# Kernel optimization log

Measured on AMD Instinct MI355X. Metric: run time of the kernel, lower is better.

## Reference

```python
import jax, jax.numpy as jnp
import numpy as np

HEAD_DIM = 64
N_HEADS = 12
ROPE_BASE = 10000.0


def _rope_tables(seq_len, head_dim, dtype=jnp.float32):
    half = head_dim // 2
    inv_freq = 1.0 / (ROPE_BASE ** (jnp.arange(0, half, dtype=jnp.float32) / half))
    pos = jnp.arange(seq_len, dtype=jnp.float32)
    freqs = pos[:, None] * inv_freq[None, :]  # (s, half)
    return jnp.cos(freqs).astype(dtype), jnp.sin(freqs).astype(dtype)


def _apply_rope(t, cos, sin):
    # t: (b, h, s, d); rotate-half convention on full head_dim (rope_fraction=1.0)
    d = t.shape[-1]
    t1, t2 = t[..., : d // 2], t[..., d // 2 :]
    cos = cos[None, None, :, :]
    sin = sin[None, None, :, :]
    return jnp.concatenate([t1 * cos - t2 * sin, t1 * sin + t2 * cos], axis=-1)


def setup_inputs() -> dict:
    key = jax.random.key(0)
    ks = jax.random.split(key, 6)
    b, s, d_model = 16, 512, 768
    x = jax.random.normal(ks[0], (b, s, d_model), dtype=jnp.float32)
    chain_ids = jax.random.randint(ks[1], (b, s), 0, 2, dtype=jnp.int32)
    attention_mask = jnp.ones((b, s), dtype=bool)
    inner = N_HEADS * HEAD_DIM
    scale = 0.02
    Wq = jax.random.normal(ks[2], (d_model, inner), dtype=jnp.float32) * scale
    Wk = jax.random.normal(ks[3], (d_model, inner), dtype=jnp.float32) * scale
    Wv = jax.random.normal(ks[4], (d_model, inner), dtype=jnp.float32) * scale
    Wo = jax.random.normal(ks[5], (inner, d_model), dtype=jnp.float32) * scale
    return {"x": x, "chain_ids": chain_ids, "attention_mask": attention_mask,
            "Wq": Wq, "Wk": Wk, "Wv": Wv, "Wo": Wo}


def reference(x, chain_ids, attention_mask, Wq, Wk, Wv, Wo):
    b, s, _ = x.shape
    h, d = N_HEADS, HEAD_DIM
    scale = d ** (-0.5)

    def proj(W):
        return jnp.einsum('bse,ef->bsf', x, W).reshape(b, s, h, d).transpose(0, 2, 1, 3)

    q = proj(Wq)  # (b, h, s, d)
    k = proj(Wk)
    v = proj(Wv)

    cos, sin = _rope_tables(s, d, x.dtype)
    q_rope = _apply_rope(q, cos, sin)
    k_rope = _apply_rope(k, cos, sin)

    scores_intra = jnp.einsum('bhsd,bhtd->bhst', q_rope, k_rope) * scale
    scores_inter = jnp.einsum('bhsd,bhtd->bhst', q, k) * scale

    # intra-chain mask (b, 1, s, s)
    intra = (chain_ids[:, None, :, None] == chain_ids[:, None, None, :])
    merged = jnp.where(intra, scores_intra, scores_inter)

    # additive padding mask (b, 1, 1, s)
    pad = jnp.where(attention_mask[:, None, None, :], 0.0, -jnp.inf).astype(x.dtype)
    merged = merged + pad

    attn = jax.nn.softmax(merged, axis=-1)
    attn = jnp.nan_to_num(attn, nan=0.0)

    out = jnp.einsum('bhst,bhtd->bhsd', attn, v)
    out = out.transpose(0, 2, 1, 3).reshape(b, s, h * d)
    return jnp.einsum('bsf,fe->bse', out, Wo)
```

## Files before the change

kernel.cpp:

```cpp
#include <hip/hip_runtime.h>
#include <stdint.h>
#include <math.h>

#define NB 16
#define NS 512
#define NH 12
#define ND 64
#define NE 768
#define NF 768

typedef __attribute__((ext_vector_type(4))) float  f32x4;
typedef __attribute__((ext_vector_type(8))) short  bf16x8;
typedef __attribute__((ext_vector_type(4))) short  bf16x4;

#define AS1(p) ((const __attribute__((address_space(1))) unsigned int*)(p))
#define AS3(p) ((__attribute__((address_space(3))) unsigned int*)(p))

__device__ __forceinline__ short f2bf(float f) {
    unsigned u = __builtin_bit_cast(unsigned, f);
    u += 0x7FFFu + ((u >> 16) & 1u);
    return (short)(u >> 16);
}
__device__ __forceinline__ float bf2f(short s) {
    unsigned u = ((unsigned)(unsigned short)s) << 16;
    return __builtin_bit_cast(float, u);
}
__device__ __forceinline__ unsigned pkbf2(float a, float b) {
    return (unsigned)(unsigned short)f2bf(a) | ((unsigned)(unsigned short)f2bf(b) << 16);
}

#define MFMA16(a, b, c) __builtin_amdgcn_mfma_f32_16x16x32_bf16((a), (b), (c), 0, 0, 0)

__device__ __forceinline__ bf16x8 lds_rd8(const short* base, int row, int cb) {
    return *(const bf16x8*)((const char*)base + (((row) * 128 + (cb)) ^ (((row) & 7) << 4)));
}

__global__ __launch_bounds__(256) void prep_kernel(float* __restrict__ cos_t,
                                                   float* __restrict__ sin_t,
                                                   const unsigned char* __restrict__ m,
                                                   int* __restrict__ flag) {
    if (blockIdx.x == 64) {
        __shared__ int any;
        if (threadIdx.x == 0) any = 0;
        __syncthreads();
        int acc = 0;
        for (int i = threadIdx.x; i < NB * NS; i += 256)
            if ((i & 3) && m[i]) acc = 1;
        if (acc) atomicOr(&any, 1);
        __syncthreads();
        if (threadIdx.x == 0) *flag = any;
        return;
    }
    int i = blockIdx.x * 256 + threadIdx.x;
    int p = i >> 5, j = i & 31;
    float inv_freq = powf(10000.0f, -(float)j / 32.0f);
    float ang = (float)p * inv_freq;
    cos_t[i] = cosf(ang);
    sin_t[i] = sinf(ang);
}

__global__ __launch_bounds__(256) void convert_x_kernel(const float* __restrict__ x,
                                                        short* __restrict__ xb) {
    int i = (blockIdx.x * 256 + threadIdx.x) * 8;
    if (i >= 8192 * 768) return;
    float4 a = *(const float4*)&x[i];
    float4 b = *(const float4*)&x[i + 4];
    bf16x8 r = { f2bf(a.x), f2bf(a.y), f2bf(a.z), f2bf(a.w),
                 f2bf(b.x), f2bf(b.y), f2bf(b.z), f2bf(b.w) };
    *(bf16x8*)&xb[i] = r;
}

__global__ __launch_bounds__(256) void convert_wt_kernel(
    const float* __restrict__ Wq, const float* __restrict__ Wk,
    const float* __restrict__ Wv, const float* __restrict__ Wo,
    short* __restrict__ Wqt, short* __restrict__ Wkt,
    short* __restrict__ Wvt, short* __restrict__ Wot) {
    const float* W  = (blockIdx.z == 0) ? Wq  : (blockIdx.z == 1) ? Wk  : (blockIdx.z == 2) ? Wv  : Wo;
    short*       Wt = (blockIdx.z == 0) ? Wqt : (blockIdx.z == 1) ? Wkt : (blockIdx.z == 2) ? Wvt : Wot;
    const int k0 = blockIdx.y * 64, n0 = blockIdx.x * 64;
    __shared__ float t[64][65];
    for (int u = threadIdx.x; u < 4096; u += 256) {
        int r = u >> 6, c = u & 63;
        t[r][c] = W[(size_t)(k0 + r) * 768 + n0 + c];
    }
    __syncthreads();
    for (int u = threadIdx.x; u < 4096; u += 256) {
        int c = u >> 6, r = u & 63;
        Wt[(size_t)(n0 + c) * 768 + k0 + r] = f2bf(t[r][c]);
    }
}

__global__ __launch_bounds__(256) void gemm_qkv_kernel(const short* __restrict__ xb,
    const short* __restrict__ Wqt, const short* __restrict__ Wkt, const short* __restrict__ Wvt,
    const float* __restrict__ cos_t, const float* __restrict__ sin_t,
    short* __restrict__ qo, short* __restrict__ ko, short* __restrict__ kpo,
    short* __restrict__ vto) {
    const int id = blockIdx.x;
    const int xcd = id & 7, rest = id >> 3;
    const int mq = rest / 18;
    const int nz = rest % 18;
    const int z  = nz / 6;
    const int n0 = (nz % 6) * 128;
    const int m0 = (xcd * 16 + mq) * 64;
    const short* Bt = (z == 0) ? Wqt : (z == 1) ? Wkt : Wvt;
    short*       O  = (z == 0) ? qo  : (z == 1) ? ko  : vto;
    __shared__ short As[2][64 * 64], Bs[2][128 * 64];
    const int tid = threadIdx.x, lane = tid & 63, wave = tid >> 6;
    const int g = lane >> 4, l15 = lane & 15;
    const int wm = wave >> 1, wn = wave & 1;
    f32x4 acc[2][4];
    #pragma unroll
    for (int i = 0; i < 2; ++i)
        #pragma unroll
        for (int j = 0; j < 4; ++j) acc[i][j] = (f32x4){0.f, 0.f, 0.f, 0.f};

    auto STAGE = [&](short* Ad, short* Bd, int kt) {
        const char* Asrc = (const char*)(xb + (size_t)m0 * 768 + kt * 64);
        const char* Bsrc = (const char*)(Bt + (size_t)n0 * 768 + kt * 64);
        #pragma unroll
        for (int p = 0; p < 2; ++p) {
            int dstoff = (wave * 2 + p) * 1024;
            int off = dstoff + lane * 16;
            int row = off >> 7, slot = off & 127;
            int srcs = slot ^ ((row & 7) << 4);
            __builtin_amdgcn_global_load_lds(AS1(Asrc + (size_t)row * 1536 + srcs),
                                             AS3((char*)Ad + dstoff), 16, 0, 0);
        }
        #pragma unroll
        for (int p = 0; p < 4; ++p) {
            int dstoff = (wave * 4 + p) * 1024;
            int off = dstoff + lane * 16;
            int row = off >> 7, slot = off & 127;
            int srcs = slot ^ ((row & 7) << 4);
            __builtin_amdgcn_global_load_lds(AS1(Bsrc + (size_t)row * 1536 + srcs),
                                             AS3((char*)Bd + dstoff), 16, 0, 0);
        }
    };
    auto COMPUTE = [&](const short* Asb, const short* Bsb) {
        __builtin_amdgcn_s_setprio(1);
        #pragma unroll
        for (int h2 = 0; h2 < 2; ++h2) {
            bf16x8 af[2], bfr[4];
            const int cb = h2 * 64 + g * 16;
            #pragma unroll
            for (int i = 0; i < 2; ++i)
                af[i]  = lds_rd8(Asb, wm * 32 + i * 16 + l15, cb);
            #pragma unroll
            for (int j = 0; j < 4; ++j)
                bfr[j] = lds_rd8(Bsb, wn * 64 + j * 16 + l15, cb);
            #pragma unroll
            for (int i = 0; i < 2; ++i)
                #pragma unroll
                for (int j = 0; j < 4; ++j)
                    acc[i][j] = MFMA16(af[i], bfr[j], acc[i][j]);
        }
        __builtin_amdgcn_s_setprio(0);
    };

    STAGE(As[0], Bs[0], 0);
    asm volatile("s_waitcnt vmcnt(0)" ::: "memory");
    __builtin_amdgcn_s_barrier();
    int cur = 0;
    for (int kt = 0; kt < 11; ++kt) {
        STAGE(As[cur ^ 1], Bs[cur ^ 1], kt + 1);
        COMPUTE(As[cur], Bs[cur]);
        asm volatile("s_waitcnt vmcnt(0)" ::: "memory");
        __builtin_amdgcn_s_barrier();
        cur ^= 1;
    }
    COMPUTE(As[cur], Bs[cur]);

    const int hh = (n0 + wn * 64) >> 6;
    #pragma unroll
    for (int i = 0; i < 2; ++i)
        #pragma unroll
        for (int r = 0; r < 4; ++r) {
            int mm = m0 + wm * 32 + i * 16 + g * 4 + r;
            int bb = mm >> 9, ss = mm & 511;
            if (z == 2) {
                #pragma unroll
                for (int j = 0; j < 4; ++j) {
                    int dd = j * 16 + l15;
                    O[(((size_t)bb * NH + hh) * ND + dd) * NS + ss] = f2bf(acc[i][j][r]);
                }
            } else {
                size_t base = (((size_t)bb * NH + hh) * NS + ss) * ND;
                #pragma unroll
                for (int j = 0; j < 4; ++j)
                    O[base + j * 16 + l15] = f2bf(acc[i][j][r]);
                if (z == 1) {
                    #pragma unroll
                    for (int p2 = 0; p2 < 2; ++p2) {
                        int jf = p2 * 16 + l15;
                        float c = cos_t[ss * 32 + jf], s = sin_t[ss * 32 + jf];
                        float t1 = acc[i][p2][r], t2 = acc[i][p2 + 2][r];
                        kpo[base + jf]      = f2bf(t1 * c - t2 * s);
                        kpo[base + 32 + jf] = f2bf(t1 * s + t2 * c);
                    }
                }
            }
        }
}

__global__ __launch_bounds__(256) void attn_fused_kernel(
    const short* __restrict__ qr, const short* __restrict__ kr, const short* __restrict__ kp,
    const short* __restrict__ vt,
    const float* __restrict__ cos_t, const float* __restrict__ sin_t,
    const int* __restrict__ chain, const void* __restrict__ amask,
    const int* __restrict__ mflag, short* __restrict__ aout) {
    const int lid = blockIdx.x;
    const int xcd = lid & 7, idx = lid >> 3;
    const int qt = idx & 7, bhl = idx >> 3;
    const int bh = xcd * 24 + bhl;
    const int b = bh / 12, h = bh - (bh / 12) * 12;
    const int q0 = qt * 64;

    __shared__ short Kr_s[4096];
    __shared__ short Kp_s[4096];
    __shared__ short Vt_s[4096];
    __shared__ short P_s[4096];
    __shared__ int   ck_a[512];
    __shared__ float kb_a[512];

    const int tid = threadIdx.x, lane = tid & 63, wave = tid >> 6;
    const int g = lane >> 4, l15 = lane & 15;
    const int m_u8 = *mflag;
    const size_t bhNS = (size_t)bh * NS;
    const float SC = 0.18033688011f;

    for (int u = tid; u < NS; u += 256) {
        int gidx = b * NS + u;
        ck_a[u] = chain[gidx];
        int ok = m_u8 ? (int)((const unsigned char*)amask)[gidx] : ((const int*)amask)[gidx];
        kb_a[u] = ok ? 0.f : -INFINITY;
    }
    const char* qrsC = (const char*)(qr + (bhNS + q0) * ND);
    #pragma unroll
    for (int p = 0; p < 2; ++p) {
        int dstoff = (wave * 2 + p) * 1024;
        int off = dstoff + lane * 16;
        int row = off >> 7, slot = off & 127;
        int srcs = slot ^ ((row & 7) << 4);
        __builtin_amdgcn_global_load_lds(AS1(qrsC + (size_t)row * 128 + srcs),
                                         AS3((char*)Kr_s + dstoff), 16, 0, 0);
    }
    __syncthreads();
    const int qrow = wave * 16 + l15;
    bf16x8 fqr0 = lds_rd8(Kr_s, qrow, g * 16);
    bf16x8 fqr1 = lds_rd8(Kr_s, qrow, 64 + g * 16);
    bf16x8 fqp0, fqp1;
    {
        int pos = q0 + qrow;
        float4 c0 = *(const float4*)&cos_t[pos * 32 + g * 8];
        float4 c1 = *(const float4*)&cos_t[pos * 32 + g * 8 + 4];
        float4 s0 = *(const float4*)&sin_t[pos * 32 + g * 8];
        float4 s1 = *(const float4*)&sin_t[pos * 32 + g * 8 + 4];
        float cc[8] = {c0.x, c0.y, c0.z, c0.w, c1.x, c1.y, c1.z, c1.w};
        float ss[8] = {s0.x, s0.y, s0.z, s0.w, s1.x, s1.y, s1.z, s1.w};
        #pragma unroll
        for (int j = 0; j < 8; ++j) {
            float t1 = bf2f(fqr0[j]), t2 = bf2f(fqr1[j]);
            fqp0[j] = f2bf(t1 * cc[j] - t2 * ss[j]);
            fqp1[j] = f2bf(t1 * ss[j] + t2 * cc[j]);
        }
    }
    const int cqv = ck_a[q0 + qrow];

    float m_run = -INFINITY, l_run = 0.f;
    f32x4 accO[4];
    #pragma unroll
    for (int t = 0; t < 4; ++t) accO[t] = (f32x4){0.f, 0.f, 0.f, 0.f};

    const char* krC = (const char*)(kr + bhNS * ND);
    const char* kpC = (const char*)(kp + bhNS * ND);
    const char* vtC = (const char*)(vt + bhNS * ND);

    for (int kv = 0; kv < 8; ++kv) {
        const int k0s = kv * 64;
        __syncthreads();
        #pragma unroll
        for (int p = 0; p < 2; ++p) {
            int dstoff = (wave * 2 + p) * 1024;
            int off = dstoff + lane * 16;
            int row = off >> 7, slot = off & 127;
            int srcs = slot ^ ((row & 7) << 4);
            size_t koff = (size_t)(k0s + row) * 128 + srcs;
            __builtin_amdgcn_global_load_lds(AS1(krC + koff), AS3((char*)Kr_s + dstoff), 16, 0, 0);
            __builtin_amdgcn_global_load_lds(AS1(kpC + koff), AS3((char*)Kp_s + dstoff), 16, 0, 0);
            __builtin_amdgcn_global_load_lds(AS1(vtC + (size_t)row * 1024 + k0s * 2 + srcs),
                                             AS3((char*)Vt_s + dstoff), 16, 0, 0);
        }
        __syncthreads();

        float pm[4][4];
        float tm = -INFINITY;
        __builtin_amdgcn_s_setprio(1);
        #pragma unroll
        for (int t = 0; t < 4; ++t) {
            bf16x8 akr0 = lds_rd8(Kr_s, t * 16 + l15, g * 16);
            bf16x8 akr1 = lds_rd8(Kr_s, t * 16 + l15, 64 + g * 16);
            bf16x8 akp0 = lds_rd8(Kp_s, t * 16 + l15, g * 16);
            bf16x8 akp1 = lds_rd8(Kp_s, t * 16 + l15, 64 + g * 16);
            f32x4 sr = (f32x4){0.f, 0.f, 0.f, 0.f};
            f32x4 sp = (f32x4){0.f, 0.f, 0.f, 0.f};
            sr = MFMA16(akr0, fqr0, sr);
            sr = MFMA16(akr1, fqr1, sr);
            sp = MFMA16(akp0, fqp0, sp);
            sp = MFMA16(akp1, fqp1, sp);
            int4   ck4 = *(const int4*)&ck_a[k0s + t * 16 + g * 4];
            float4 kb4 = *(const float4*)&kb_a[k0s + t * 16 + g * 4];
            const int   ckk[4] = {ck4.x, ck4.y, ck4.z, ck4.w};
            const float kbb[4] = {kb4.x, kb4.y, kb4.z, kb4.w};
            #pragma unroll
            for (int r = 0; r < 4; ++r) {
                float sv = (cqv == ckk[r]) ? sp[r] : sr[r];
                sv = sv * SC + kbb[r];
                pm[t][r] = sv;
                tm = fmaxf(tm, sv);
            }
        }
        __builtin_amdgcn_s_setprio(0);

        tm = fmaxf(tm, __shfl_xor(tm, 16));
        tm = fmaxf(tm, __shfl_xor(tm, 32));
        bool skip = __all(tm - m_run <= 8.f);
        float mnew, fac;
        if (skip) { mnew = m_run; fac = 1.f; }
        else      { mnew = fmaxf(m_run, tm); fac = exp2f(m_run - mnew); }
        float psum = 0.f;
        if (mnew == -INFINITY) {
            #pragma unroll
            for (int t = 0; t < 4; ++t)
                #pragma unroll
                for (int r = 0; r < 4; ++r) pm[t][r] = 0.f;
            fac = 1.f;
        } else {
            #pragma unroll
            for (int t = 0; t < 4; ++t)
                #pragma unroll
                for (int r = 0; r < 4; ++r) {
                    float p = exp2f(pm[t][r] - mnew);
                    pm[t][r] = p;
                    psum += p;
                }
        }
        psum += __shfl_xor(psum, 16);
        psum += __shfl_xor(psum, 32);
        l_run = l_run * fac + psum;
        m_run = mnew;

        char* pwave = (char*)P_s + wave * 2048;
        int psw = (l15 & 7) << 4;
        #pragma unroll
        for (int t = 0; t < 4; ++t) {
            unsigned u0 = pkbf2(pm[t][0], pm[t][1]);
            unsigned u1 = pkbf2(pm[t][2], pm[t][3]);
            uint2 pk = {u0, u1};
            *(uint2*)(pwave + ((l15 * 128 + t * 32 + g * 8) ^ psw)) = pk;
        }
        if (!skip) {
            float f4[4];
            #pragma unroll
            for (int r = 0; r < 4; ++r) f4[r] = __shfl(fac, g * 4 + r);
            #pragma unroll
            for (int t = 0; t < 4; ++t) {
                f32x4 a = accO[t];
                a[0] *= f4[0]; a[1] *= f4[1]; a[2] *= f4[2]; a[3] *= f4[3];
                accO[t] = a;
            }
        }
        bf16x8 pa0 = *(const bf16x8*)(pwave + ((l15 * 128 + g * 16) ^ psw));
        bf16x8 pa1 = *(const bf16x8*)(pwave + ((l15 * 128 + 64 + g * 16) ^ psw));
        __builtin_amdgcn_s_setprio(1);
        #pragma unroll
        for (int dt = 0; dt < 4; ++dt) {
            bf16x8 vb0 = lds_rd8(Vt_s, dt * 16 + l15, g * 16);
            bf16x8 vb1 = lds_rd8(Vt_s, dt * 16 + l15, 64 + g * 16);
            accO[dt] = MFMA16(pa0, vb0, accO[dt]);
            accO[dt] = MFMA16(pa1, vb1, accO[dt]);
        }
        __builtin_amdgcn_s_setprio(0);
    }

    float inv[4];
    #pragma unroll
    for (int r = 0; r < 4; ++r) {
        float lv = __shfl(l_run, g * 4 + r);
        inv[r] = (lv > 0.f) ? 1.f / lv : 0.f;
    }
    #pragma unroll
    for (int dt = 0; dt < 4; ++dt)
        #pragma unroll
        for (int r = 0; r < 4; ++r) {
            int row = b * NS + q0 + wave * 16 + g * 4 + r;
            aout[(size_t)row * NF + h * ND + dt * 16 + l15] = f2bf(accO[dt][r] * inv[r]);
        }
}

__global__ __launch_bounds__(256) void gemm_out_kernel(const short* __restrict__ A,
    const short* __restrict__ Wot, float* __restrict__ out) {
    const int id = blockIdx.x;
    const int xcd = id & 7, rest = id >> 3;
    const int mq = rest / 6;
    const int n0 = (rest % 6) * 128;
    const int m0 = (xcd * 16 + mq) * 64;
    __shared__ short As[2][64 * 64], Bs[2][128 * 64];
    const int tid = threadIdx.x, lane = tid & 63, wave = tid >> 6;
    const int g = lane >> 4, l15 = lane & 15;
    const int wm = wave >> 1, wn = wave & 1;
    f32x4 acc[2][4];
    #pragma unroll
    for (int i = 0; i < 2; ++i)
        #pragma unroll
        for (int j = 0; j < 4; ++j) acc[i][j] = (f32x4){0.f, 0.f, 0.f, 0.f};

    auto STAGE = [&](short* Ad, short* Bd, int kt) {
        const char* Asrc = (const char*)(A   + (size_t)m0 * 768 + kt * 64);
        const char* Bsrc = (const char*)(Wot + (size_t)n0 * 768 + kt * 64);
        #pragma unroll
        for (int p = 0; p < 2; ++p) {
            int dstoff = (wave * 2 + p) * 1024;
            int off = dstoff + lane * 16;
            int row = off >> 7, slot = off & 127;
            int srcs = slot ^ ((row & 7) << 4);
            __builtin_amdgcn_global_load_lds(AS1(Asrc + (size_t)row * 1536 + srcs),
                                             AS3((char*)Ad + dstoff), 16, 0, 0);
        }
        #pragma unroll
        for (int p = 0; p < 4; ++p) {
            int dstoff = (wave * 4 + p) * 1024;
            int off = dstoff + lane * 16;
            int row = off >> 7, slot = off & 127;
            int srcs = slot ^ ((row & 7) << 4);
            __builtin_amdgcn_global_load_lds(AS1(Bsrc + (size_t)row * 1536 + srcs),
                                             AS3((char*)Bd + dstoff), 16, 0, 0);
        }
    };
    auto COMPUTE = [&](const short* Asb, const short* Bsb) {
        __builtin_amdgcn_s_setprio(1);
        #pragma unroll
        for (int h2 = 0; h2 < 2; ++h2) {
            bf16x8 af[2], bfr[4];
            const int cb = h2 * 64 + g * 16;
            #pragma unroll
            for (int i = 0; i < 2; ++i)
                af[i]  = lds_rd8(Asb, wm * 32 + i * 16 + l15, cb);
            #pragma unroll
            for (int j = 0; j < 4; ++j)
                bfr[j] = lds_rd8(Bsb, wn * 64 + j * 16 + l15, cb);
            #pragma unroll
            for (int i = 0; i < 2; ++i)
                #pragma unroll
                for (int j = 0; j < 4; ++j)
                    acc[i][j] = MFMA16(af[i], bfr[j], acc[i][j]);
        }
        __builtin_amdgcn_s_setprio(0);
    };

    STAGE(As[0], Bs[0], 0);
    asm volatile("s_waitcnt vmcnt(0)" ::: "memory");
    __builtin_amdgcn_s_barrier();
    int cur = 0;
    for (int kt = 0; kt < 11; ++kt) {
        STAGE(As[cur ^ 1], Bs[cur ^ 1], kt + 1);
        COMPUTE(As[cur], Bs[cur]);
        asm volatile("s_waitcnt vmcnt(0)" ::: "memory");
        __builtin_amdgcn_s_barrier();
        cur ^= 1;
    }
    COMPUTE(As[cur], Bs[cur]);

    #pragma unroll
    for (int i = 0; i < 2; ++i)
        #pragma unroll
        for (int r = 0; r < 4; ++r) {
            int mm = m0 + wm * 32 + i * 16 + g * 4 + r;
            #pragma unroll
            for (int j = 0; j < 4; ++j) {
                int n = n0 + wn * 64 + j * 16 + l15;
                out[(size_t)mm * NE + n] = acc[i][j][r];
            }
        }
}

extern "C" void kernel_launch(void* const* d_in, const int* in_sizes, int n_in,
                              void* d_out, int out_size, void* d_ws, size_t ws_size,
                              hipStream_t stream) {
    const float* x     = (const float*)d_in[0];
    const int*   chain = (const int*)d_in[1];
    const void*  amask = d_in[2];
    const float* Wq = (const float*)d_in[3];
    const float* Wk = (const float*)d_in[4];
    const float* Wv = (const float*)d_in[5];
    const float* Wo = (const float*)d_in[6];
    float* out = (float*)d_out;

    const size_t QSZ = (size_t)NB * NH * NS * ND;
    char* w = (char*)d_ws;
    float* cos_t = (float*)w;  w += (size_t)NS * 32 * 4;
    float* sin_t = (float*)w;  w += (size_t)NS * 32 * 4;
    int*   mflag = (int*)w;    w += 256;
    short* xb    = (short*)w;  w += (size_t)8192 * 768 * 2;
    short* Wqt   = (short*)w;  w += (size_t)768 * 768 * 2;
    short* Wkt   = (short*)w;  w += (size_t)768 * 768 * 2;
    short* Wvt   = (short*)w;  w += (size_t)768 * 768 * 2;
    short* Wot   = (short*)w;  w += (size_t)768 * 768 * 2;
    short* q_raw = (short*)w;  w += QSZ * 2;
    short* k_raw = (short*)w;  w += QSZ * 2;
    short* k_rop = (short*)w;  w += QSZ * 2;
    short* vtr   = (short*)w;  w += QSZ * 2;
    short* aout  = xb;

    prep_kernel<<<dim3(65), dim3(256), 0, stream>>>(cos_t, sin_t,
                                                    (const unsigned char*)amask, mflag);
    convert_x_kernel<<<dim3(3072), dim3(256), 0, stream>>>(x, xb);
    convert_wt_kernel<<<dim3(12, 12, 4), dim3(256), 0, stream>>>(Wq, Wk, Wv, Wo, Wqt, Wkt, Wvt, Wot);
    gemm_qkv_kernel<<<dim3(2304), dim3(256), 0, stream>>>(xb, Wqt, Wkt, Wvt, cos_t, sin_t,
                                                          q_raw, k_raw, k_rop, vtr);
    attn_fused_kernel<<<dim3(1536), dim3(256), 0, stream>>>(q_raw, k_raw, k_rop, vtr,
                                                            cos_t, sin_t, chain, amask, mflag, aout);
    gemm_out_kernel<<<dim3(768), dim3(256), 0, stream>>>(aout, Wot, out);
}
```

Measured before the change: 157.2 us.

## Merge prep kernels into one launch and enlarge QKV GEMM M tile

Folds the rope-table, mask-flag, weight-transpose and x-conversion kernels into a single launch partitioned by block index, cutting two launches. The QKV GEMM tile grows from 64x128 to 128x128 per block, with four waves each computing 64x64, which halves the grid and raises operand reuse per LDS load. The cost is more accumulator registers and LDS per block, which may reduce occupancy.

```diff
diff --git a/kernel.cpp b/kernel.cpp
--- a/kernel.cpp
+++ b/kernel.cpp
@@ -11,7 +11,6 @@
 
 typedef __attribute__((ext_vector_type(4))) float  f32x4;
 typedef __attribute__((ext_vector_type(8))) short  bf16x8;
-typedef __attribute__((ext_vector_type(4))) short  bf16x4;
 
 #define AS1(p) ((const __attribute__((address_space(1))) unsigned int*)(p))
 #define AS3(p) ((__attribute__((address_space(3))) unsigned int*)(p))
@@ -35,11 +34,25 @@
     return *(const bf16x8*)((const char*)base + (((row) * 128 + (cb)) ^ (((row) & 7) << 4)));
 }
 
-__global__ __launch_bounds__(256) void prep_kernel(float* __restrict__ cos_t,
-                                                   float* __restrict__ sin_t,
-                                                   const unsigned char* __restrict__ m,
-                                                   int* __restrict__ flag) {
-    if (blockIdx.x == 64) {
+__global__ __launch_bounds__(256) void prep_all_kernel(
+    const float* __restrict__ x, short* __restrict__ xb,
+    const float* __restrict__ Wq, const float* __restrict__ Wk,
+    const float* __restrict__ Wv, const float* __restrict__ Wo,
+    short* __restrict__ Wqt, short* __restrict__ Wkt,
+    short* __restrict__ Wvt, short* __restrict__ Wot,
+    float* __restrict__ cos_t, float* __restrict__ sin_t,
+    const unsigned char* __restrict__ m, int* __restrict__ flag) {
+    const int bid = blockIdx.x;
+    if (bid < 64) {
+        int i = bid * 256 + threadIdx.x;
+        int p = i >> 5, j = i & 31;
+        float inv_freq = powf(10000.0f, -(float)j / 32.0f);
+        float ang = (float)p * inv_freq;
+        cos_t[i] = cosf(ang);
+        sin_t[i] = sinf(ang);
+        return;
+    }
+    if (bid == 64) {
         __shared__ int any;
         if (threadIdx.x == 0) any = 0;
         __syncthreads();
@@ -51,43 +64,30 @@
         if (threadIdx.x == 0) *flag = any;
         return;
     }
-    int i = blockIdx.x * 256 + threadIdx.x;
-    int p = i >> 5, j = i & 31;
-    float inv_freq = powf(10000.0f, -(float)j / 32.0f);
-    float ang = (float)p * inv_freq;
-    cos_t[i] = cosf(ang);
-    sin_t[i] = sinf(ang);
-}
-
-__global__ __launch_bounds__(256) void convert_x_kernel(const float* __restrict__ x,
-                                                        short* __restrict__ xb) {
-    int i = (blockIdx.x * 256 + threadIdx.x) * 8;
-    if (i >= 8192 * 768) return;
+    if (bid < 641) {
+        int idx = bid - 65;
+        int zz = idx / 144, r2 = idx % 144;
+        const float* W  = (zz == 0) ? Wq  : (zz == 1) ? Wk  : (zz == 2) ? Wv  : Wo;
+        short*       Wt = (zz == 0) ? Wqt : (zz == 1) ? Wkt : (zz == 2) ? Wvt : Wot;
+        const int k0 = (r2 / 12) * 64, n0 = (r2 % 12) * 64;
+        __shared__ float t[64][65];
+        for (int u = threadIdx.x; u < 4096; u += 256) {
+            int r = u >> 6, c = u & 63;
+            t[r][c] = W[(size_t)(k0 + r) * 768 + n0 + c];
+        }
+        __syncthreads();
+        for (int u = threadIdx.x; u < 4096; u += 256) {
+            int c = u >> 6, r = u & 63;
+            Wt[(size_t)(n0 + c) * 768 + k0 + r] = f2bf(t[r][c]);
+        }
+        return;
+    }
+    int i = ((bid - 641) * 256 + threadIdx.x) * 8;
     float4 a = *(const float4*)&x[i];
     float4 b = *(const float4*)&x[i + 4];
     bf16x8 r = { f2bf(a.x), f2bf(a.y), f2bf(a.z), f2bf(a.w),
                  f2bf(b.x), f2bf(b.y), f2bf(b.z), f2bf(b.w) };
     *(bf16x8*)&xb[i] = r;
-}
-
-__global__ __launch_bounds__(256) void convert_wt_kernel(
-    const float* __restrict__ Wq, const float* __restrict__ Wk,
-    const float* __restrict__ Wv, const float* __restrict__ Wo,
-    short* __restrict__ Wqt, short* __restrict__ Wkt,
-    short* __restrict__ Wvt, short* __restrict__ Wot) {
-    const float* W  = (blockIdx.z == 0) ? Wq  : (blockIdx.z == 1) ? Wk  : (blockIdx.z == 2) ? Wv  : Wo;
-    short*       Wt = (blockIdx.z == 0) ? Wqt : (blockIdx.z == 1) ? Wkt : (blockIdx.z == 2) ? Wvt : Wot;
-    const int k0 = blockIdx.y * 64, n0 = blockIdx.x * 64;
-    __shared__ float t[64][65];
-    for (int u = threadIdx.x; u < 4096; u += 256) {
-        int r = u >> 6, c = u & 63;
-        t[r][c] = W[(size_t)(k0 + r) * 768 + n0 + c];
-    }
-    __syncthreads();
-    for (int u = threadIdx.x; u < 4096; u += 256) {
-        int c = u >> 6, r = u & 63;
-        Wt[(size_t)(n0 + c) * 768 + k0 + r] = f2bf(t[r][c]);
-    }
 }
 
 __global__ __launch_bounds__(256) void gemm_qkv_kernel(const short* __restrict__ xb,
@@ -101,16 +101,16 @@
     const int nz = rest % 18;
     const int z  = nz / 6;
     const int n0 = (nz % 6) * 128;
-    const int m0 = (xcd * 16 + mq) * 64;
+    const int m0 = (xcd * 8 + mq) * 128;
     const short* Bt = (z == 0) ? Wqt : (z == 1) ? Wkt : Wvt;
     short*       O  = (z == 0) ? qo  : (z == 1) ? ko  : vto;
-    __shared__ short As[2][64 * 64], Bs[2][128 * 64];
+    __shared__ short As[2][128 * 64], Bs[2][128 * 64];
     const int tid = threadIdx.x, lane = tid & 63, wave = tid >> 6;
     const int g = lane >> 4, l15 = lane & 15;
     const int wm = wave >> 1, wn = wave & 1;
-    f32x4 acc[2][4];
-    #pragma unroll
-    for (int i = 0; i < 2; ++i)
+    f32x4 acc[4][4];
+    #pragma unroll
+    for (int i = 0; i < 4; ++i)
         #pragma unroll
         for (int j = 0; j < 4; ++j) acc[i][j] = (f32x4){0.f, 0.f, 0.f, 0.f};
 
@@ -118,20 +118,13 @@
         const char* Asrc = (const char*)(xb + (size_t)m0 * 768 + kt * 64);
         const char* Bsrc = (const char*)(Bt + (size_t)n0 * 768 + kt * 64);
         #pragma unroll
-        for (int p = 0; p < 2; ++p) {
-            int dstoff = (wave * 2 + p) * 1024;
+        for (int p = 0; p < 4; ++p) {
+            int dstoff = (wave * 4 + p) * 1024;
             int off = dstoff + lane * 16;
             int row = off >> 7, slot = off & 127;
             int srcs = slot ^ ((row & 7) << 4);
             __builtin_amdgcn_global_load_lds(AS1(Asrc + (size_t)row * 1536 + srcs),
                                              AS3((char*)Ad + dstoff), 16, 0, 0);
-        }
-        #pragma unroll
-        for (int p = 0; p < 4; ++p) {
-            int dstoff = (wave * 4 + p) * 1024;
-            int off = dstoff + lane * 16;
-            int row = off >> 7, slot = off & 127;
-            int srcs = slot ^ ((row & 7) << 4);
             __builtin_amdgcn_global_load_lds(AS1(Bsrc + (size_t)row * 1536 + srcs),
                                              AS3((char*)Bd + dstoff), 16, 0, 0);
         }
@@ -140,16 +133,15 @@
         __builtin_amdgcn_s_setprio(1);
         #pragma unroll
         for (int h2 = 0; h2 < 2; ++h2) {
-            bf16x8 af[2], bfr[4];
+            bf16x8 af[4], bfr[4];
             const int cb = h2 * 64 + g * 16;
             #pragma unroll
-            for (int i = 0; i < 2; ++i)
-                af[i]  = lds_rd8(Asb, wm * 32 + i * 16 + l15, cb);
-            #pragma unroll
-            for (int j = 0; j < 4; ++j)
-                bfr[j] = lds_rd8(Bsb, wn * 64 + j * 16 + l15, cb);
-            #pragma unroll
-            for (int i = 0; i < 2; ++i)
+            for (int i = 0; i < 4; ++i) {
+                af[i]  = lds_rd8(Asb, wm * 64 + i * 16 + l15, cb);
+                bfr[i] = lds_rd8(Bsb, wn * 64 + i * 16 + l15, cb);
+            }
+            #pragma unroll
+            for (int i = 0; i < 4; ++i)
                 #pragma unroll
                 for (int j = 0; j < 4; ++j)
                     acc[i][j] = MFMA16(af[i], bfr[j], acc[i][j]);
@@ -172,10 +164,10 @@
 
     const int hh = (n0 + wn * 64) >> 6;
     #pragma unroll
-    for (int i = 0; i < 2; ++i)
+    for (int i = 0; i < 4; ++i)
         #pragma unroll
         for (int r = 0; r < 4; ++r) {
-            int mm = m0 + wm * 32 + i * 16 + g * 4 + r;
+            int mm = m0 + wm * 64 + i * 16 + g * 4 + r;
             int bb = mm >> 9, ss = mm & 511;
             if (z == 2) {
                 #pragma unroll
@@ -511,11 +503,11 @@
     short* vtr   = (short*)w;  w += QSZ * 2;
     short* aout  = xb;
 
-    prep_kernel<<<dim3(65), dim3(256), 0, stream>>>(cos_t, sin_t,
-                                                    (const unsigned char*)amask, mflag);
-    convert_x_kernel<<<dim3(3072), dim3(256), 0, stream>>>(x, xb);
-    convert_wt_kernel<<<dim3(12, 12, 4), dim3(256), 0, stream>>>(Wq, Wk, Wv, Wo, Wqt, Wkt, Wvt, Wot);
-    gemm_qkv_kernel<<<dim3(2304), dim3(256), 0, stream>>>(xb, Wqt, Wkt, Wvt, cos_t, sin_t,
+    prep_all_kernel<<<dim3(3713), dim3(256), 0, stream>>>(x, xb, Wq, Wk, Wv, Wo,
+                                                          Wqt, Wkt, Wvt, Wot,
+                                                          cos_t, sin_t,
+                                                          (const unsigned char*)amask, mflag);
+    gemm_qkv_kernel<<<dim3(1152), dim3(256), 0, stream>>>(xb, Wqt, Wkt, Wvt, cos_t, sin_t,
                                                           q_raw, k_raw, k_rop, vtr);
     attn_fused_kernel<<<dim3(1536), dim3(256), 0, stream>>>(q_raw, k_raw, k_rop, vtr,
                                                             cos_t, sin_t, chain, amask, mflag, aout);
```

Result: faster. 152.2 us (-3.2%).
